# Optimization experiments

Measured on AMD Instinct MI355X. Metric: run time of the kernel, lower is better.

Reference implementation:

```python
import jax, jax.numpy as jnp
import numpy as np

ENT_SIZE = 250000
REL_SIZE = 64
EMBED = 128
B = 32768
K = 8


def setup_inputs() -> dict:
    key = jax.random.key(0)
    ks = jax.random.split(key, 9)
    initrange = 0.5 / EMBED
    u = lambda k, n: jax.random.uniform(k, (n, EMBED), jnp.float32, -initrange, initrange)
    V = ENT_SIZE + REL_SIZE  # unified vocab: entities first, then relations
    return {
        "in_ent_w": u(ks[0], ENT_SIZE),
        "out_ent_w": u(ks[1], ENT_SIZE),
        "in_rel_w": u(ks[2], REL_SIZE),
        "out_rel_w": u(ks[3], REL_SIZE),
        "in_map_w": u(ks[4], REL_SIZE),
        "out_map_w": u(ks[5], REL_SIZE),
        "input_labels": jax.random.randint(ks[6], (B,), 0, V, jnp.int32),
        "pos_labels": jax.random.randint(ks[7], (B,), 0, V, jnp.int32),
        "neg_labels": jax.random.randint(ks[8], (B, K), 0, V, jnp.int32),
    }


def _map(ent, mapping):
    # project ent onto the hyperplane normal to normalize(mapping)  (TransH-style)
    n = mapping / jnp.maximum(jnp.linalg.norm(mapping, axis=-1, keepdims=True), 1e-12)
    return ent - jnp.sum(ent * n, axis=-1, keepdims=True) * n


def _pair_embs(iid, pid, is_ent_i, is_ent_p, in_ent_w, out_ent_w, in_rel_w, out_rel_w, in_map_w, out_map_w):
    """Per-row (input_emb, output_emb) per the 4 mask branches, plus the stable
    permutation that reproduces torch's boolean-mask + concat row ordering."""
    rel_size = in_rel_w.shape[0]
    iid_r = jnp.minimum(iid, rel_size - 1)  # clip: only used where label is a relation
    pid_r = jnp.minimum(pid, rel_size - 1)
    e_in = in_ent_w[iid]        # [N, D]
    r_in = in_rel_w[iid_r]
    e_out = out_ent_w[pid]
    r_out = out_rel_w[pid_r]
    mp_in = in_map_w[pid_r]
    mp_out = out_map_w[iid_r]
    mi = is_ent_i[:, None]
    mp = is_ent_p[:, None]
    inp = jnp.where(mi, jnp.where(mp, e_in, _map(e_in, mp_in)), r_in)
    out = jnp.where(mp, jnp.where(mi, e_out, _map(e_out, mp_out)), r_out)
    # branch key: 0=(ent,ent) 1=(ent,rel) 2=(rel,ent) 3=(rel,rel) -> concat order
    branch = (~is_ent_i).astype(jnp.int32) * 2 + (~is_ent_p).astype(jnp.int32)
    perm = jnp.argsort(branch, stable=True)
    return inp[perm], out[perm]


def reference(in_ent_w, out_ent_w, in_rel_w, out_rel_w, in_map_w, out_map_w,
              input_labels, pos_labels, neg_labels):
    ent_size = in_ent_w.shape[0]
    b, k = neg_labels.shape
    neg_flat = neg_labels.reshape(-1)

    # reverse_id_map: entity labels keep id, relation labels offset by ent_size
    to_id = lambda lab: jnp.where(lab < ent_size, lab, lab - ent_size)
    is_ent = lambda lab: lab < ent_size

    iid, pid, nid = to_id(input_labels), to_id(pos_labels), to_id(neg_flat)
    ii, ip, inn = is_ent(input_labels), is_ent(pos_labels), is_ent(neg_flat)

    Ws = (in_ent_w, out_ent_w, in_rel_w, out_rel_w, in_map_w, out_map_w)

    inp_pos, out_pos = _pair_embs(iid, pid, ii, ip, *Ws)
    iid_rep = jnp.repeat(iid, k)
    ii_rep = jnp.repeat(ii, k)
    inp_neg, out_neg = _pair_embs(iid_rep, nid, ii_rep, inn, *Ws)

    log_pos = jax.nn.log_sigmoid(jnp.sum(out_pos * inp_pos, axis=-1))          # [B]
    log_neg = jax.nn.log_sigmoid(jnp.sum(out_neg * (-inp_neg), axis=-1))       # [B*K]
    log_neg = log_neg.reshape(b, k).sum(axis=1)                                # [B]
    return -(log_pos + log_neg)
```

## Files before the change

### kernel.cpp

```cpp
#include <hip/hip_runtime.h>
#include <hip/hip_bf16.h>
#include <stdint.h>

#define ENT 250000
#define RELSZ 64
#define D 128
#define BATCH 32768
#define KNEG 8

#define CAPP 2048
#define CAPN 6144


__device__ __forceinline__ float logsig(float x) {
  return fminf(x, 0.f) - log1pf(expf(-fabsf(x)));
}

__global__ void k_prep(const float* __restrict__ in_rel, const float* __restrict__ out_rel,
                       const float* __restrict__ in_map, const float* __restrict__ out_map,
                       const int* __restrict__ in_lab, const int* __restrict__ pos_lab,
                       const int* __restrict__ neg_lab,
                       float* __restrict__ t1, float* __restrict__ t2, float* __restrict__ RR,
                       int* __restrict__ U_pos, int* __restrict__ U_neg,
                       int* __restrict__ gcnt, float* __restrict__ out) {
  __shared__ float ls[4];
  __shared__ float sri[2][128];
  int blk = blockIdx.x, t = threadIdx.x;

  if (blk < 32) {
    int sub = t >> 7, tt = t & 127;
    int p = blk * 2 + sub;
    float im = in_map[p * D + tt], om = out_map[p * D + tt];
    float ro = out_rel[p * D + tt], ri = in_rel[p * D + tt];
    float v, r, n_im, n_om;
    v = im * im;
#pragma unroll
    for (int off = 32; off > 0; off >>= 1) v += __shfl_xor(v, off, 64);
    if ((t & 63) == 0) ls[t >> 6] = v;
    __syncthreads();
    r = ls[sub * 2] + ls[sub * 2 + 1];
    n_im = im / fmaxf(sqrtf(r), 1e-12f);
    __syncthreads();
    v = om * om;
#pragma unroll
    for (int off = 32; off > 0; off >>= 1) v += __shfl_xor(v, off, 64);
    if ((t & 63) == 0) ls[t >> 6] = v;
    __syncthreads();
    r = ls[sub * 2] + ls[sub * 2 + 1];
    n_om = om / fmaxf(sqrtf(r), 1e-12f);
    __syncthreads();
    v = n_im * ro;
#pragma unroll
    for (int off = 32; off > 0; off >>= 1) v += __shfl_xor(v, off, 64);
    if ((t & 63) == 0) ls[t >> 6] = v;
    __syncthreads();
    float d1 = ls[sub * 2] + ls[sub * 2 + 1];
    __syncthreads();
    v = n_om * ri;
#pragma unroll
    for (int off = 32; off > 0; off >>= 1) v += __shfl_xor(v, off, 64);
    if ((t & 63) == 0) ls[t >> 6] = v;
    __syncthreads();
    float d2 = ls[sub * 2] + ls[sub * 2 + 1];
    t1[p * D + tt] = ro - d1 * n_im;
    t2[p * D + tt] = ri - d2 * n_om;
    sri[sub][tt] = ri;
    __syncthreads();
    int half = t >> 7, lq = t & 127;
    if (lq < RELSZ) {
      int pr = blk * 2 + half;
      const float* rq = out_rel + lq * D;
      const float* s = sri[half];
      float acc = 0.f;
#pragma unroll 8
      for (int d = 0; d < D; d += 4) {
        float4 r4 = *(const float4*)(rq + d);
        acc += s[d] * r4.x + s[d + 1] * r4.y + s[d + 2] * r4.z + s[d + 3] * r4.w;
      }
      RR[pr * RELSZ + lq] = acc;
    }
    return;
  }

  if (blk < 64) {
    int idx = (blk - 32) * 256 + t;
    ((float4*)out)[idx] = make_float4(0.f, 0.f, 0.f, 0.f);
    return;
  }

  int row = (blk - 64) * 256 + t;
  int il = in_lab[row], pl = pos_lab[row];
  int kb = (il >= ENT) ? 2 : 0;
  int kp = kb | ((pl >= ENT) ? 1 : 0);
  int4 n0 = *(const int4*)(neg_lab + row * 8);
  int4 n1 = *(const int4*)(neg_lab + row * 8 + 4);
  int k0 = kb | ((n0.x >= ENT) ? 1 : 0), k1 = kb | ((n0.y >= ENT) ? 1 : 0);
  int k2 = kb | ((n0.z >= ENT) ? 1 : 0), k3 = kb | ((n0.w >= ENT) ? 1 : 0);
  int k4 = kb | ((n1.x >= ENT) ? 1 : 0), k5 = kb | ((n1.y >= ENT) ? 1 : 0);
  int k6 = kb | ((n1.z >= ENT) ? 1 : 0), k7 = kb | ((n1.w >= ENT) ? 1 : 0);
  bool has = (kp | k0 | k1 | k2 | k3 | k4 | k5 | k6 | k7) != 0;
  if (__ballot(has) == 0ull) return;
  if (has) {
    if (kp) { int s = atomicAdd(gcnt, 1); if (s < CAPP) U_pos[s] = (row << 2) | kp; }
    int kv[8] = {k0, k1, k2, k3, k4, k5, k6, k7};
#pragma unroll
    for (int j = 0; j < 8; j++)
      if (kv[j]) {
        int s = atomicAdd(gcnt + 1, 1);
        if (s < CAPN) U_neg[s] = ((row * 8 + j) << 2) | kv[j];
      }
  }
}

__global__ void k_sort(const int* __restrict__ U_pos, const int* __restrict__ U_neg,
                       const int* __restrict__ gcnt, int* __restrict__ hdr,
                       int* __restrict__ E_pos, int* __restrict__ D_pos,
                       int* __restrict__ E_neg, int* __restrict__ D_neg) {
  __shared__ int vp[CAPP];
  __shared__ int vn[CAPN];
  __shared__ int ckey[8];
  int t = threadIdx.x;
  int np = min(gcnt[0], CAPP), nn = min(gcnt[1], CAPN);
  if (t < 8) ckey[t] = 0;
  __syncthreads();
  for (int j = t; j < np; j += 256) vp[j] = U_pos[j];
  for (int j = t; j < nn; j += 256) vn[j] = U_neg[j];
  __syncthreads();
  for (int j = t; j < np; j += 256) atomicAdd(&ckey[vp[j] & 3], 1);
  for (int j = t; j < nn; j += 256) atomicAdd(&ckey[4 + (vn[j] & 3)], 1);
  __syncthreads();
  int c1 = ckey[1], c2 = ckey[2], c3 = ckey[3];
  int N0p = BATCH - c1 - c2 - c3;
  int d1 = ckey[5], d2 = ckey[6], d3 = ckey[7];
  int N0n = BATCH * KNEG - d1 - d2 - d3;
  for (int j = t; j < np; j += 256) {
    int v = vp[j], key = v & 3;
    int r = 0, rk = 0;
    for (int m = 0; m < np; m++) {
      int u = vp[m];
      r += (u < v) ? 1 : 0;
      rk += ((u < v) && ((u & 3) == key)) ? 1 : 0;
    }
    int bbase = (key == 1) ? N0p : (key == 2) ? N0p + c1 : N0p + c1 + c2;
    E_pos[r] = v >> 2;
    D_pos[r] = bbase + rk;
  }
  for (int j = t; j < nn; j += 256) {
    int v = vn[j], key = v & 3;
    int r = 0, rk = 0;
    for (int m = 0; m < nn; m++) {
      int u = vn[m];
      r += (u < v) ? 1 : 0;
      rk += ((u < v) && ((u & 3) == key)) ? 1 : 0;
    }
    int bbase = (key == 1) ? N0n : (key == 2) ? N0n + d1 : N0n + d1 + d2;
    E_neg[r] = v >> 2;
    D_neg[r] = bbase + rk;
  }
  if (t == 0) { hdr[0] = np; hdr[1] = nn; }
}

__global__ void __launch_bounds__(256, 4)
k_main(const float* __restrict__ in_ent, const float* __restrict__ out_ent,
       const float* __restrict__ t1, const float* __restrict__ t2,
       const float* __restrict__ RR,
       const int* __restrict__ in_lab, const int* __restrict__ pos_lab,
       const int* __restrict__ neg_lab,
       const int* __restrict__ hdr,
       const int* __restrict__ E_pos, const int* __restrict__ D_pos,
       const int* __restrict__ E_neg, const int* __restrict__ D_neg,
       float* __restrict__ out) {
  int blk = blockIdx.x, t = threadIdx.x;
  int wave = t >> 6, lane = t & 63;
  int q = lane & 3, g = lane >> 2;

  bool is_pos = blk < 512;
  int w = (is_pos ? blk : blk - 512) * 4 + wave;
  int i = w * 16 + g;

  int il, o;
  if (is_pos) { il = in_lab[i]; o = pos_lab[i]; }
  else        { il = in_lab[i >> 3]; o = neg_lab[i]; }
  bool ei = il < ENT;
  int iid = ei ? il : il - ENT;
  bool eo = o < ENT;
  int oid = eo ? o : o - ENT;
  int key = (ei ? 0 : 2) | (eo ? 0 : 1);

  const float* Lp = (ei ? in_ent + (size_t)iid * D : t2 + (size_t)iid * D) + q * 4;
  const float* Rp = (eo ? out_ent + (size_t)oid * D : t1 + (size_t)oid * D) + q * 4;
  float4 L[8], R[8];
#pragma unroll
  for (int k = 0; k < 8; k++) L[k] = *(const float4*)(Lp + k * 16);
#pragma unroll
  for (int k = 0; k < 8; k++) R[k] = *(const float4*)(Rp + k * 16);

  int n = is_pos ? hdr[0] : hdr[1];
  const int* E = is_pos ? E_pos : E_neg;
  int lo = 0, hi = n;
  while (lo < hi) {
    int mid = (lo + hi) >> 1;
    bool lt = E[mid] < i;
    lo = lt ? mid + 1 : lo;
    hi = lt ? hi : mid;
  }
  int s = (key == 0) ? (i - lo) : (is_pos ? D_pos[lo] : D_neg[lo]);

  float p = 0.f;
#pragma unroll
  for (int k = 0; k < 8; k++)
    p += L[k].x * R[k].x + L[k].y * R[k].y + L[k].z * R[k].z + L[k].w * R[k].w;
  p += __shfl_xor(p, 1, 64);
  p += __shfl_xor(p, 2, 64);

  float dot = p;
  if (!ei && !eo) dot = RR[iid * RELSZ + oid];

  if (is_pos) {
    if (q == 0) atomicAdd(out + s, -logsig(dot));
    return;
  }

  int dest = s >> 3;
  float myval = (q == 0) ? -logsig(-dot) : 0.f;
  float v = myval;
  int d = dest;
  int eq = 1;
#pragma unroll
  for (int off = 4; off <= 16; off <<= 1) {
    float vv = __shfl_xor(v, off, 64);
    int dd = __shfl_xor(d, off, 64);
    int ee = __shfl_xor(eq, off, 64);
    eq = eq & ee & (dd == d ? 1 : 0);
    v += vv;
  }
  if (eq) {
    if (lane == 0 || lane == 32) atomicAdd(out + d, v);
  } else if (q == 0) {
    atomicAdd(out + dest, myval);
  }
}

extern "C" void kernel_launch(void* const* d_in, const int* in_sizes, int n_in,
                              void* d_out, int out_size, void* d_ws, size_t ws_size,
                              hipStream_t stream) {
  const float* in_ent  = (const float*)d_in[0];
  const float* out_ent = (const float*)d_in[1];
  const float* in_rel  = (const float*)d_in[2];
  const float* out_rel = (const float*)d_in[3];
  const float* in_map  = (const float*)d_in[4];
  const float* out_map = (const float*)d_in[5];
  const int* in_lab  = (const int*)d_in[6];
  const int* pos_lab = (const int*)d_in[7];
  const int* neg_lab = (const int*)d_in[8];

  char* ws = (char*)d_ws;
  float* t1    = (float*)(ws + 0);
  float* t2    = (float*)(ws + 32768);
  float* RR    = (float*)(ws + 65536);
  int*   hdr   = (int*)(ws + 81920);
  int*   E_pos = (int*)(ws + 82176);
  int*   D_pos = (int*)(ws + 90368);
  int*   E_neg = (int*)(ws + 98560);
  int*   D_neg = (int*)(ws + 123136);
  int*   U_pos = (int*)(ws + 147712);
  int*   U_neg = (int*)(ws + 155904);
  int*   gcnt  = (int*)(ws + 180480);
  float* out   = (float*)d_out;

  hipMemsetAsync(gcnt, 0, 8, stream);
  k_prep<<<192, 256, 0, stream>>>(in_rel, out_rel, in_map, out_map,
                                  in_lab, pos_lab, neg_lab,
                                  t1, t2, RR, U_pos, U_neg, gcnt, out);
  k_sort<<<1, 256, 0, stream>>>(U_pos, U_neg, gcnt, hdr, E_pos, D_pos, E_neg, D_neg);
  k_main<<<4608, 256, 0, stream>>>(in_ent, out_ent, t1, t2, RR,
                                   in_lab, pos_lab, neg_lab,
                                   hdr, E_pos, D_pos, E_neg, D_neg, out);
}
```

Baseline: 54.33 us.

## Replace global atomics with per-block shared compaction and drop the counter memset

Each label-scanning block now compacts its non-entity rows into shared memory with shared atomics, then writes them to a per-block slot in global memory along with per-block counts. The sort kernel gathers these per-block lists with one thread per block. This removes contended global atomics and the separate memset launch. In exchange, the gather in the sort kernel is serial per block, and the workspace layout grows.

Measured after the change: 52.25 us. -3.8%, faster.

```diff
diff --git a/kernel.cpp b/kernel.cpp
--- a/kernel.cpp
+++ b/kernel.cpp
@@ -22,9 +22,13 @@
                        const int* __restrict__ neg_lab,
                        float* __restrict__ t1, float* __restrict__ t2, float* __restrict__ RR,
                        int* __restrict__ U_pos, int* __restrict__ U_neg,
-                       int* __restrict__ gcnt, float* __restrict__ out) {
+                       int* __restrict__ cntp, int* __restrict__ cntn,
+                       float* __restrict__ out) {
   __shared__ float ls[4];
   __shared__ float sri[2][128];
+  __shared__ int sp[256];
+  __shared__ int sn[2048];
+  __shared__ int sc[2];
   int blk = blockIdx.x, t = threadIdx.x;
 
   if (blk < 32) {
@@ -88,7 +92,10 @@
     return;
   }
 
-  int row = (blk - 64) * 256 + t;
+  if (t < 2) sc[t] = 0;
+  __syncthreads();
+  int bb = blk - 64;
+  int row = bb * 256 + t;
   int il = in_lab[row], pl = pos_lab[row];
   int kb = (il >= ENT) ? 2 : 0;
   int kp = kb | ((pl >= ENT) ? 1 : 0);
@@ -99,38 +106,52 @@
   int k4 = kb | ((n1.x >= ENT) ? 1 : 0), k5 = kb | ((n1.y >= ENT) ? 1 : 0);
   int k6 = kb | ((n1.z >= ENT) ? 1 : 0), k7 = kb | ((n1.w >= ENT) ? 1 : 0);
   bool has = (kp | k0 | k1 | k2 | k3 | k4 | k5 | k6 | k7) != 0;
-  if (__ballot(has) == 0ull) return;
   if (has) {
-    if (kp) { int s = atomicAdd(gcnt, 1); if (s < CAPP) U_pos[s] = (row << 2) | kp; }
+    if (kp) { int s = atomicAdd(&sc[0], 1); sp[s] = (row << 2) | kp; }
     int kv[8] = {k0, k1, k2, k3, k4, k5, k6, k7};
 #pragma unroll
     for (int j = 0; j < 8; j++)
-      if (kv[j]) {
-        int s = atomicAdd(gcnt + 1, 1);
-        if (s < CAPN) U_neg[s] = ((row * 8 + j) << 2) | kv[j];
-      }
-  }
+      if (kv[j]) { int s = atomicAdd(&sc[1], 1); sn[s] = ((row * 8 + j) << 2) | kv[j]; }
+  }
+  __syncthreads();
+  int np = sc[0], nn = sc[1];
+  for (int j = t; j < np; j += 256) U_pos[bb * 256 + j] = sp[j];
+  for (int j = t; j < nn; j += 256) U_neg[bb * 2048 + j] = sn[j];
+  if (t == 0) { cntp[bb] = np; cntn[bb] = nn; }
 }
 
 __global__ void k_sort(const int* __restrict__ U_pos, const int* __restrict__ U_neg,
-                       const int* __restrict__ gcnt, int* __restrict__ hdr,
+                       const int* __restrict__ cntp, const int* __restrict__ cntn,
+                       int* __restrict__ hdr,
                        int* __restrict__ E_pos, int* __restrict__ D_pos,
                        int* __restrict__ E_neg, int* __restrict__ D_neg) {
   __shared__ int vp[CAPP];
   __shared__ int vn[CAPN];
+  __shared__ int c2[2];
   __shared__ int ckey[8];
   int t = threadIdx.x;
-  int np = min(gcnt[0], CAPP), nn = min(gcnt[1], CAPN);
+  if (t < 2) c2[t] = 0;
   if (t < 8) ckey[t] = 0;
   __syncthreads();
-  for (int j = t; j < np; j += 256) vp[j] = U_pos[j];
-  for (int j = t; j < nn; j += 256) vn[j] = U_neg[j];
-  __syncthreads();
+  for (int b = t; b < 128; b += 256) {
+    int cp = cntp[b];
+    if (cp > 0) {
+      int base = atomicAdd(&c2[0], cp);
+      for (int j = 0; j < cp && base + j < CAPP; j++) vp[base + j] = U_pos[b * 256 + j];
+    }
+    int cn = cntn[b];
+    if (cn > 0) {
+      int base = atomicAdd(&c2[1], cn);
+      for (int j = 0; j < cn && base + j < CAPN; j++) vn[base + j] = U_neg[b * 2048 + j];
+    }
+  }
+  __syncthreads();
+  int np = min(c2[0], CAPP), nn = min(c2[1], CAPN);
   for (int j = t; j < np; j += 256) atomicAdd(&ckey[vp[j] & 3], 1);
   for (int j = t; j < nn; j += 256) atomicAdd(&ckey[4 + (vn[j] & 3)], 1);
   __syncthreads();
-  int c1 = ckey[1], c2 = ckey[2], c3 = ckey[3];
-  int N0p = BATCH - c1 - c2 - c3;
+  int c1 = ckey[1], cc2 = ckey[2], c3 = ckey[3];
+  int N0p = BATCH - c1 - cc2 - c3;
   int d1 = ckey[5], d2 = ckey[6], d3 = ckey[7];
   int N0n = BATCH * KNEG - d1 - d2 - d3;
   for (int j = t; j < np; j += 256) {
@@ -141,7 +162,7 @@
       r += (u < v) ? 1 : 0;
       rk += ((u < v) && ((u & 3) == key)) ? 1 : 0;
     }
-    int bbase = (key == 1) ? N0p : (key == 2) ? N0p + c1 : N0p + c1 + c2;
+    int bbase = (key == 1) ? N0p : (key == 2) ? N0p + c1 : N0p + c1 + cc2;
     E_pos[r] = v >> 2;
     D_pos[r] = bbase + rk;
   }
@@ -263,16 +284,17 @@
   int*   D_pos = (int*)(ws + 90368);
   int*   E_neg = (int*)(ws + 98560);
   int*   D_neg = (int*)(ws + 123136);
-  int*   U_pos = (int*)(ws + 147712);
-  int*   U_neg = (int*)(ws + 155904);
-  int*   gcnt  = (int*)(ws + 180480);
+  int*   cntp  = (int*)(ws + 147712);
+  int*   cntn  = (int*)(ws + 148224);
+  int*   U_pos = (int*)(ws + 148736);
+  int*   U_neg = (int*)(ws + 279808);
   float* out   = (float*)d_out;
 
-  hipMemsetAsync(gcnt, 0, 8, stream);
   k_prep<<<192, 256, 0, stream>>>(in_rel, out_rel, in_map, out_map,
                                   in_lab, pos_lab, neg_lab,
-                                  t1, t2, RR, U_pos, U_neg, gcnt, out);
-  k_sort<<<1, 256, 0, stream>>>(U_pos, U_neg, gcnt, hdr, E_pos, D_pos, E_neg, D_neg);
+                                  t1, t2, RR, U_pos, U_neg, cntp, cntn, out);
+  k_sort<<<1, 256, 0, stream>>>(U_pos, U_neg, cntp, cntn, hdr,
+                                E_pos, D_pos, E_neg, D_neg);
   k_main<<<4608, 256, 0, stream>>>(in_ent, out_ent, t1, t2, RR,
                                    in_lab, pos_lab, neg_lab,
                                    hdr, E_pos, D_pos, E_neg, D_neg, out);
```
